# Kernel optimization log

Hardware: AMD Instinct MI355X
Metric: run time of the kernel (lower is better)

Reference implementation:

```python
import jax, jax.numpy as jnp
import numpy as np

# SMPL kinematic tree parents (joint 0 is root)
SMPL_PARENTS = [-1, 0, 0, 0, 1, 2, 3, 4, 5, 6, 7, 8, 9, 9, 9, 12, 13, 14, 16, 17, 18, 19, 20, 21]
NUM_JOINTS = 24


def _rodrigues(axisang):
    # axisang: (B, J, 3) -> (B, J, 3, 3), matching th_posemap_axisang's eps handling
    angle = jnp.linalg.norm(axisang + 1e-8, axis=-1, keepdims=True)  # (B,J,1)
    axis = axisang / angle
    a = angle[..., None]                      # (B,J,1,1)
    c, s = jnp.cos(a), jnp.sin(a)
    x, y, z = axis[..., 0], axis[..., 1], axis[..., 2]
    zero = jnp.zeros_like(x)
    # skew-symmetric cross-product matrix K
    K = jnp.stack([
        jnp.stack([zero, -z, y], axis=-1),
        jnp.stack([z, zero, -x], axis=-1),
        jnp.stack([-y, x, zero], axis=-1),
    ], axis=-2)                               # (B,J,3,3)
    outer = axis[..., :, None] * axis[..., None, :]
    eye = jnp.eye(3, dtype=axisang.dtype)
    return c * eye + (1.0 - c) * outer + s * K


def setup_inputs() -> dict:
    key = jax.random.key(0)
    k1, k2, k3 = jax.random.split(key, 3)
    B, N = 16, 100000
    normals = jax.random.normal(k1, (B, 3, N), dtype=jnp.float32)
    pose = jax.random.normal(k2, (B, 72), dtype=jnp.float32)
    skinning_weights = jax.random.uniform(k3, (B, NUM_JOINTS, N), dtype=jnp.float32)
    return {"normals": normals, "pose": pose, "skinning_weights": skinning_weights}


def reference(normals, pose, skinning_weights):
    B = pose.shape[0]
    rots = _rodrigues(pose.reshape(B, NUM_JOINTS, 3))  # (B,24,3,3)
    # sequential kinematic-chain composition over the fixed 24-joint tree
    results = [rots[:, 0]]
    for i in range(1, NUM_JOINTS):
        results.append(jnp.matmul(results[SMPL_PARENTS[i]], rots[:, i]))
    th_results2 = jnp.stack(results, axis=-1)          # (B,3,3,24)
    # skinning: (B,9,24) @ (B,24,N) -> (B,3,3,N)
    n_T = jnp.einsum('bijk,bkn->bijn', th_results2, skinning_weights)
    # rotate normals: sum over local axis j of n_T[b,i,j,n] * normals[b,j,n]
    n_verts = jnp.einsum('bijn,bjn->bin', n_T, normals)  # (B,3,N)
    return n_verts
```

## Files before the change

kernel.cpp:

```cpp
#include <hip/hip_runtime.h>

#define NUM_JOINTS 24

typedef float fvec4 __attribute__((ext_vector_type(4)));

__device__ __constant__ int d_chain[NUM_JOINTS][9] = {
    {0,-1,-1,-1,-1,-1,-1,-1,-1},
    {0,1,-1,-1,-1,-1,-1,-1,-1},
    {0,2,-1,-1,-1,-1,-1,-1,-1},
    {0,3,-1,-1,-1,-1,-1,-1,-1},
    {0,1,4,-1,-1,-1,-1,-1,-1},
    {0,2,5,-1,-1,-1,-1,-1,-1},
    {0,3,6,-1,-1,-1,-1,-1,-1},
    {0,1,4,7,-1,-1,-1,-1,-1},
    {0,2,5,8,-1,-1,-1,-1,-1},
    {0,3,6,9,-1,-1,-1,-1,-1},
    {0,1,4,7,10,-1,-1,-1,-1},
    {0,2,5,8,11,-1,-1,-1,-1},
    {0,3,6,9,12,-1,-1,-1,-1},
    {0,3,6,9,13,-1,-1,-1,-1},
    {0,3,6,9,14,-1,-1,-1,-1},
    {0,3,6,9,12,15,-1,-1,-1},
    {0,3,6,9,13,16,-1,-1,-1},
    {0,3,6,9,14,17,-1,-1,-1},
    {0,3,6,9,13,16,18,-1,-1},
    {0,3,6,9,14,17,19,-1,-1},
    {0,3,6,9,13,16,18,20,-1},
    {0,3,6,9,14,17,19,21,-1},
    {0,3,6,9,13,16,18,20,22},
    {0,3,6,9,14,17,19,21,23},
};

__device__ __forceinline__ fvec4 fma4s(fvec4 a, float s, fvec4 c) {
    fvec4 r;
    r.x = fmaf(a.x, s, c.x); r.y = fmaf(a.y, s, c.y);
    r.z = fmaf(a.z, s, c.z); r.w = fmaf(a.w, s, c.w);
    return r;
}
__device__ __forceinline__ fvec4 fma4v(fvec4 a, fvec4 b, fvec4 c) {
    fvec4 r;
    r.x = fmaf(a.x, b.x, c.x); r.y = fmaf(a.y, b.y, c.y);
    r.z = fmaf(a.z, b.z, c.z); r.w = fmaf(a.w, b.w, c.w);
    return r;
}
__device__ __forceinline__ fvec4 mul4s(fvec4 a, float s) {
    fvec4 r; r.x = a.x * s; r.y = a.y * s; r.z = a.z * s; r.w = a.w * s;
    return r;
}

#define PF 8

__global__ __launch_bounds__(256) void skin_fused4_kernel(
    const float* __restrict__ normals,
    const float* __restrict__ pose,
    const float* __restrict__ weights,
    float* __restrict__ out,
    int N) {
    __shared__ float L[NUM_JOINTS][9];
    __shared__ fvec4 Rl[NUM_JOINTS][3];

    const int b = blockIdx.y;
    const int tid = threadIdx.x;

    if (tid < NUM_JOINTS) {
        float x = pose[b * 72 + tid * 3 + 0];
        float y = pose[b * 72 + tid * 3 + 1];
        float z = pose[b * 72 + tid * 3 + 2];
        float ax = x + 1e-8f, ay = y + 1e-8f, az = z + 1e-8f;
        float angle = sqrtf(ax * ax + ay * ay + az * az);
        float inv = 1.0f / angle;
        float ux = x * inv, uy = y * inv, uz = z * inv;
        float c = __cosf(angle), s = __sinf(angle), t = 1.0f - c;
        L[tid][0] = c + t * ux * ux;
        L[tid][1] = t * ux * uy - s * uz;
        L[tid][2] = t * ux * uz + s * uy;
        L[tid][3] = t * uy * ux + s * uz;
        L[tid][4] = c + t * uy * uy;
        L[tid][5] = t * uy * uz - s * ux;
        L[tid][6] = t * uz * ux - s * uy;
        L[tid][7] = t * uz * uy + s * ux;
        L[tid][8] = c + t * uz * uz;
    }
    __syncthreads();

    if (tid < NUM_JOINTS) {
        float G[9];
        int j0 = d_chain[tid][0];
        #pragma unroll
        for (int e = 0; e < 9; e++) G[e] = L[j0][e];
        #pragma unroll
        for (int d = 1; d < 9; d++) {
            int j = d_chain[tid][d];
            if (j >= 0) {
                float T[9];
                #pragma unroll
                for (int r = 0; r < 3; r++) {
                    #pragma unroll
                    for (int cc = 0; cc < 3; cc++) {
                        T[r * 3 + cc] = G[r * 3 + 0] * L[j][0 * 3 + cc]
                                      + G[r * 3 + 1] * L[j][1 * 3 + cc]
                                      + G[r * 3 + 2] * L[j][2 * 3 + cc];
                    }
                }
                #pragma unroll
                for (int e = 0; e < 9; e++) G[e] = T[e];
            }
        }
        float* Rf = (float*)Rl;
        #pragma unroll
        for (int e = 0; e < 9; e++) Rf[tid * 12 + e] = G[e];
    }
    __syncthreads();

    const int q = blockIdx.x * blockDim.x + tid;
    const int nf4 = N >> 2;

    const fvec4* __restrict__ Wb = (const fvec4*)(weights + (size_t)b * NUM_JOINTS * N);
    const fvec4* __restrict__ Nb = (const fvec4*)(normals + (size_t)b * 3 * N);
    fvec4* __restrict__ Ob = (fvec4*)(out + (size_t)b * 3 * N);

    if (q < nf4) {
        fvec4 nx = __builtin_nontemporal_load(&Nb[(size_t)0 * nf4 + q]);
        fvec4 ny = __builtin_nontemporal_load(&Nb[(size_t)1 * nf4 + q]);
        fvec4 nz = __builtin_nontemporal_load(&Nb[(size_t)2 * nf4 + q]);

        fvec4 w[PF];
        #pragma unroll
        for (int j = 0; j < PF; j++)
            w[j] = __builtin_nontemporal_load(&Wb[(size_t)j * nf4 + q]);

        fvec4 o0 = (fvec4)(0.f), o1 = (fvec4)(0.f), o2 = (fvec4)(0.f);

        #pragma unroll
        for (int k = 0; k < NUM_JOINTS; k++) {
            fvec4 wk = w[k & (PF - 1)];
            if (k + PF < NUM_JOINTS)
                w[k & (PF - 1)] =
                    __builtin_nontemporal_load(&Wb[(size_t)(k + PF) * nf4 + q]);
            fvec4 r0 = Rl[k][0];
            fvec4 r1 = Rl[k][1];
            fvec4 r2 = Rl[k][2];
            fvec4 t0 = fma4s(nx, r0.x, fma4s(ny, r0.y, mul4s(nz, r0.z)));
            fvec4 t1 = fma4s(nx, r0.w, fma4s(ny, r1.x, mul4s(nz, r1.y)));
            fvec4 t2 = fma4s(nx, r1.z, fma4s(ny, r1.w, mul4s(nz, r2.x)));
            o0 = fma4v(wk, t0, o0);
            o1 = fma4v(wk, t1, o1);
            o2 = fma4v(wk, t2, o2);
        }

        __builtin_nontemporal_store(o0, &Ob[(size_t)0 * nf4 + q]);
        __builtin_nontemporal_store(o1, &Ob[(size_t)1 * nf4 + q]);
        __builtin_nontemporal_store(o2, &Ob[(size_t)2 * nf4 + q]);
    } else if (q == nf4) {
        const float* Rf = (const float*)Rl;
        for (int n = nf4 * 4; n < N; n++) {
            float vx = normals[(size_t)b * 3 * N + 0 * N + n];
            float vy = normals[(size_t)b * 3 * N + 1 * N + n];
            float vz = normals[(size_t)b * 3 * N + 2 * N + n];
            float s0 = 0.f, s1 = 0.f, s2 = 0.f;
            for (int k = 0; k < NUM_JOINTS; k++) {
                float w = weights[(size_t)b * NUM_JOINTS * N + (size_t)k * N + n];
                float t0 = Rf[k*12+0] * vx + Rf[k*12+1] * vy + Rf[k*12+2] * vz;
                float t1 = Rf[k*12+3] * vx + Rf[k*12+4] * vy + Rf[k*12+5] * vz;
                float t2 = Rf[k*12+6] * vx + Rf[k*12+7] * vy + Rf[k*12+8] * vz;
                s0 = fmaf(w, t0, s0); s1 = fmaf(w, t1, s1); s2 = fmaf(w, t2, s2);
            }
            out[(size_t)b * 3 * N + 0 * N + n] = s0;
            out[(size_t)b * 3 * N + 1 * N + n] = s1;
            out[(size_t)b * 3 * N + 2 * N + n] = s2;
        }
    }
}

extern "C" void kernel_launch(void* const* d_in, const int* in_sizes, int n_in,
                              void* d_out, int out_size, void* d_ws, size_t ws_size,
                              hipStream_t stream) {
    const float* normals = (const float*)d_in[0];
    const float* pose = (const float*)d_in[1];
    const float* weights = (const float*)d_in[2];
    float* out = (float*)d_out;

    const int B = in_sizes[1] / 72;
    const int N = in_sizes[0] / (3 * B);

    const int nf4 = N >> 2;
    const int slots = nf4 + 1;
    const int gx = (slots + 255) / 256;
    skin_fused4_kernel<<<dim3(gx, B), dim3(256), 0, stream>>>(normals, pose, weights, out, N);
}
```

Baseline: 250.0 us.

## Use fixed balanced grid with per-block contiguous ranges and drop weight prefetch ring

Launches a fixed number of blocks (512 total split across batches) and gives each block a balanced contiguous range of float4 slots, looping threads over that range. This amortizes the per-block rotation-chain setup over more elements. The explicit 8-deep weight prefetch ring is replaced by a plain per-joint load with partial unrolling. This risks fewer memory requests in flight and lower occupancy on a bandwidth-bound kernel.

```diff
diff --git a/kernel.cpp b/kernel.cpp
--- a/kernel.cpp
+++ b/kernel.cpp
@@ -48,9 +48,7 @@
     return r;
 }
 
-#define PF 8
-
-__global__ __launch_bounds__(256) void skin_fused4_kernel(
+__global__ __launch_bounds__(256) void skin_bal4_kernel(
     const float* __restrict__ normals,
     const float* __restrict__ pose,
     const float* __restrict__ weights,
@@ -112,46 +110,46 @@
     }
     __syncthreads();
 
-    const int q = blockIdx.x * blockDim.x + tid;
     const int nf4 = N >> 2;
+    const int gx = gridDim.x;
+    const int per = nf4 / gx;
+    const int rem = nf4 - per * gx;
+    const int bx = blockIdx.x;
+    const int base = bx * per + (bx < rem ? bx : rem);
+    const int cnt = per + (bx < rem ? 1 : 0);
 
     const fvec4* __restrict__ Wb = (const fvec4*)(weights + (size_t)b * NUM_JOINTS * N);
     const fvec4* __restrict__ Nb = (const fvec4*)(normals + (size_t)b * 3 * N);
     fvec4* __restrict__ Ob = (fvec4*)(out + (size_t)b * 3 * N);
 
-    if (q < nf4) {
-        fvec4 nx = __builtin_nontemporal_load(&Nb[(size_t)0 * nf4 + q]);
-        fvec4 ny = __builtin_nontemporal_load(&Nb[(size_t)1 * nf4 + q]);
-        fvec4 nz = __builtin_nontemporal_load(&Nb[(size_t)2 * nf4 + q]);
+    for (int i = tid; i < cnt; i += 256) {
+        const int c = base + i;
 
-        fvec4 w[PF];
-        #pragma unroll
-        for (int j = 0; j < PF; j++)
-            w[j] = __builtin_nontemporal_load(&Wb[(size_t)j * nf4 + q]);
-
+        fvec4 nx = __builtin_nontemporal_load(&Nb[(size_t)0 * nf4 + c]);
+        fvec4 ny = __builtin_nontemporal_load(&Nb[(size_t)1 * nf4 + c]);
+        fvec4 nz = __builtin_nontemporal_load(&Nb[(size_t)2 * nf4 + c]);
         fvec4 o0 = (fvec4)(0.f), o1 = (fvec4)(0.f), o2 = (fvec4)(0.f);
 
-        #pragma unroll
+        #pragma unroll 4
         for (int k = 0; k < NUM_JOINTS; k++) {
-            fvec4 wk = w[k & (PF - 1)];
-            if (k + PF < NUM_JOINTS)
-                w[k & (PF - 1)] =
-                    __builtin_nontemporal_load(&Wb[(size_t)(k + PF) * nf4 + q]);
+            fvec4 w = __builtin_nontemporal_load(&Wb[(size_t)k * nf4 + c]);
             fvec4 r0 = Rl[k][0];
             fvec4 r1 = Rl[k][1];
             fvec4 r2 = Rl[k][2];
             fvec4 t0 = fma4s(nx, r0.x, fma4s(ny, r0.y, mul4s(nz, r0.z)));
             fvec4 t1 = fma4s(nx, r0.w, fma4s(ny, r1.x, mul4s(nz, r1.y)));
             fvec4 t2 = fma4s(nx, r1.z, fma4s(ny, r1.w, mul4s(nz, r2.x)));
-            o0 = fma4v(wk, t0, o0);
-            o1 = fma4v(wk, t1, o1);
-            o2 = fma4v(wk, t2, o2);
+            o0 = fma4v(w, t0, o0);
+            o1 = fma4v(w, t1, o1);
+            o2 = fma4v(w, t2, o2);
         }
 
-        __builtin_nontemporal_store(o0, &Ob[(size_t)0 * nf4 + q]);
-        __builtin_nontemporal_store(o1, &Ob[(size_t)1 * nf4 + q]);
-        __builtin_nontemporal_store(o2, &Ob[(size_t)2 * nf4 + q]);
-    } else if (q == nf4) {
+        __builtin_nontemporal_store(o0, &Ob[(size_t)0 * nf4 + c]);
+        __builtin_nontemporal_store(o1, &Ob[(size_t)1 * nf4 + c]);
+        __builtin_nontemporal_store(o2, &Ob[(size_t)2 * nf4 + c]);
+    }
+
+    if (blockIdx.x == 0 && tid == 0) {
         const float* Rf = (const float*)Rl;
         for (int n = nf4 * 4; n < N; n++) {
             float vx = normals[(size_t)b * 3 * N + 0 * N + n];
@@ -183,8 +181,7 @@
     const int B = in_sizes[1] / 72;
     const int N = in_sizes[0] / (3 * B);
 
-    const int nf4 = N >> 2;
-    const int slots = nf4 + 1;
-    const int gx = (slots + 255) / 256;
-    skin_fused4_kernel<<<dim3(gx, B), dim3(256), 0, stream>>>(normals, pose, weights, out, N);
+    int gx = 512 / B;
+    if (gx < 1) gx = 1;
+    skin_bal4_kernel<<<dim3(gx, B), dim3(256), 0, stream>>>(normals, pose, weights, out, N);
 }
```

After: 226.1 us. 9.5% less time.
